# Kernel tuning notes

Hardware: AMD Instinct MI355X
Metric: run time of the kernel (lower is better)

The kernel has to match this reference:

```python
import jax, jax.numpy as jnp
import numpy as np

OUT_C, K, Z_DIM = 256, 64 and 64, 3  # placeholder; real constants below
OUT_C = 256
K = 3
Z_DIM = 64
B, H, W = 16, 128, 128


def setup_inputs() -> dict:
    key = jax.random.key(0)
    k1, k2, k3 = jax.random.split(key, 3)
    x = jax.random.normal(k1, (B, OUT_C, H, W), dtype=jnp.float32)
    z = jax.random.normal(k2, (B, Z_DIM), dtype=jnp.float32)
    # nn.Linear(z_dim, out_c*k*k, bias=False) weight: (out_c*k*k, z_dim)
    W_lin = jax.random.normal(k3, (OUT_C * K * K, Z_DIM), dtype=jnp.float32) * 0.05
    return {"x": x, "z": z, "W_lin": W_lin}


def reference(x, z, W_lin):
    # Hypernetwork: per-sample depthwise kernels, (B, out_c, 1, k, k)
    W_dw = (z @ W_lin.T).reshape(B, OUT_C, 1, K, K)
    pad = K // 2

    def conv_one(xi, wi):
        # xi: (C,H,W), wi: (out_c,1,k,k); depthwise conv, groups=out_c==C
        return jax.lax.conv_general_dilated(
            xi[None],  # (1,C,H,W)
            wi,
            window_strides=(1, 1),
            padding=[(pad, pad), (pad, pad)],
            dimension_numbers=("NCHW", "OIHW", "NCHW"),
            feature_group_count=OUT_C,
        )[0]

    return jax.vmap(conv_one)(x, W_dw)  # (B, out_c, H, W)
```

## Files before the change

### kernel.cpp

```cpp
#include <hip/hip_runtime.h>
#include <hip/hip_bf16.h>

#define BATCH   16
#define OUT_C   256
#define KK      3
#define Z_DIM   64
#define H_DIM   128
#define W_DIM   128

typedef float vf4 __attribute__((ext_vector_type(4)));

__global__ void hyper_gemm_kernel(const float* __restrict__ z,
                                  const float* __restrict__ W_lin,
                                  float* __restrict__ wdw) {
    const int tid = blockIdx.x * blockDim.x + threadIdx.x;
    const int total = BATCH * OUT_C * KK * KK;
    if (tid >= total) return;
    const int b = tid / (OUT_C * KK * KK);
    const int j = tid - b * (OUT_C * KK * KK);

    const vf4* zr = reinterpret_cast<const vf4*>(z + b * Z_DIM);
    const vf4* wr = reinterpret_cast<const vf4*>(W_lin + (size_t)j * Z_DIM);

    float acc = 0.f;
#pragma unroll
    for (int i = 0; i < Z_DIM / 4; ++i) {
        vf4 a = zr[i];
        vf4 w = wr[i];
        acc += a.x * w.x + a.y * w.y + a.z * w.z + a.w * w.w;
    }
    wdw[tid] = acc;
}

__global__ __launch_bounds__(256)
void dwconv3x3_kernel(const float* __restrict__ x,
                      const float* __restrict__ wdw,
                      float* __restrict__ out) {
    const int slab  = blockIdx.x & 1;
    const int plane = blockIdx.x >> 1;

    const float* __restrict__ xin  = x   + (size_t)plane * (H_DIM * W_DIM);
    float*       __restrict__ oout = out + (size_t)plane * (H_DIM * W_DIM);

    const float* __restrict__ wp = wdw + (size_t)plane * (KK * KK);
    const float w00 = wp[0], w01 = wp[1], w02 = wp[2];
    const float w10 = wp[3], w11 = wp[4], w12 = wp[5];
    const float w20 = wp[6], w21 = wp[7], w22 = wp[8];

    const int tcol = threadIdx.x & 31;
    const int trow = threadIdx.x >> 5;
    const int c0   = tcol * 4;
    const int r0   = slab * 64 + trow * 8;

    vf4 raw[10];
#pragma unroll
    for (int i = 0; i < 10; ++i) {
        const int ir  = r0 - 1 + i;
        const int irc = ir < 0 ? 0 : (ir > H_DIM - 1 ? H_DIM - 1 : ir);
        raw[i] = *reinterpret_cast<const vf4*>(xin + irc * W_DIM + c0);
    }
    __builtin_amdgcn_sched_barrier(0);

    vf4   m[10];
    float lft[10], rgt[10];
#pragma unroll
    for (int i = 0; i < 10; ++i) {
        const int ir = r0 - 1 + i;
        const float msk = (ir >= 0 && ir < H_DIM) ? 1.f : 0.f;
        m[i] = raw[i] * msk;
        const float tl = __shfl_up(m[i].w, 1);
        const float tr = __shfl_down(m[i].x, 1);
        lft[i] = (tcol == 0)  ? 0.f : tl;
        rgt[i] = (tcol == 31) ? 0.f : tr;
    }

#pragma unroll
    for (int j = 0; j < 8; ++j) {
        const float A[6] = { lft[j],     m[j].x,     m[j].y,     m[j].z,     m[j].w,     rgt[j]     };
        const float B[6] = { lft[j + 1], m[j + 1].x, m[j + 1].y, m[j + 1].z, m[j + 1].w, rgt[j + 1] };
        const float C[6] = { lft[j + 2], m[j + 2].x, m[j + 2].y, m[j + 2].z, m[j + 2].w, rgt[j + 2] };

        vf4 s;
        float o[4];
#pragma unroll
        for (int k = 0; k < 4; ++k) {
            float a;
            a = fmaf(w00, A[k], fmaf(w01, A[k + 1], w02 * A[k + 2]));
            a = fmaf(w10, B[k], fmaf(w11, B[k + 1], fmaf(w12, B[k + 2], a)));
            a = fmaf(w20, C[k], fmaf(w21, C[k + 1], fmaf(w22, C[k + 2], a)));
            o[k] = a;
        }
        s.x = o[0]; s.y = o[1]; s.z = o[2]; s.w = o[3];
        __builtin_nontemporal_store(
            s, reinterpret_cast<vf4*>(oout + (r0 + j) * W_DIM + c0));
    }
}

extern "C" void kernel_launch(void* const* d_in, const int* in_sizes, int n_in,
                              void* d_out, int out_size, void* d_ws, size_t ws_size,
                              hipStream_t stream) {
    const float* x     = (const float*)d_in[0];
    const float* z     = (const float*)d_in[1];
    const float* W_lin = (const float*)d_in[2];
    float* out = (float*)d_out;
    float* wdw = (float*)d_ws;

    {
        const int total = BATCH * OUT_C * KK * KK;
        const int blk = 256;
        hyper_gemm_kernel<<<(total + blk - 1) / blk, blk, 0, stream>>>(z, W_lin, wdw);
    }

    {
        const int grid = BATCH * OUT_C * 2;
        dwconv3x3_kernel<<<grid, 256, 0, stream>>>(x, wdw, out);
    }
}
```

Before: 87.01 us.

## Fuse hypernetwork weight GEMV into depthwise conv kernel via wavefront reductions

```diff
diff --git a/kernel.cpp b/kernel.cpp
--- a/kernel.cpp
+++ b/kernel.cpp
@@ -10,42 +10,18 @@
 
 typedef float vf4 __attribute__((ext_vector_type(4)));
 
-__global__ void hyper_gemm_kernel(const float* __restrict__ z,
-                                  const float* __restrict__ W_lin,
-                                  float* __restrict__ wdw) {
-    const int tid = blockIdx.x * blockDim.x + threadIdx.x;
-    const int total = BATCH * OUT_C * KK * KK;
-    if (tid >= total) return;
-    const int b = tid / (OUT_C * KK * KK);
-    const int j = tid - b * (OUT_C * KK * KK);
-
-    const vf4* zr = reinterpret_cast<const vf4*>(z + b * Z_DIM);
-    const vf4* wr = reinterpret_cast<const vf4*>(W_lin + (size_t)j * Z_DIM);
-
-    float acc = 0.f;
-#pragma unroll
-    for (int i = 0; i < Z_DIM / 4; ++i) {
-        vf4 a = zr[i];
-        vf4 w = wr[i];
-        acc += a.x * w.x + a.y * w.y + a.z * w.z + a.w * w.w;
-    }
-    wdw[tid] = acc;
-}
-
 __global__ __launch_bounds__(256)
-void dwconv3x3_kernel(const float* __restrict__ x,
-                      const float* __restrict__ wdw,
-                      float* __restrict__ out) {
+void dwconv3x3_fused_kernel(const float* __restrict__ x,
+                            const float* __restrict__ z,
+                            const float* __restrict__ W_lin,
+                            float* __restrict__ out) {
     const int slab  = blockIdx.x & 1;
     const int plane = blockIdx.x >> 1;
+    const int b     = plane >> 8;
+    const int c     = plane & 255;
 
     const float* __restrict__ xin  = x   + (size_t)plane * (H_DIM * W_DIM);
     float*       __restrict__ oout = out + (size_t)plane * (H_DIM * W_DIM);
-
-    const float* __restrict__ wp = wdw + (size_t)plane * (KK * KK);
-    const float w00 = wp[0], w01 = wp[1], w02 = wp[2];
-    const float w10 = wp[3], w11 = wp[4], w12 = wp[5];
-    const float w20 = wp[6], w21 = wp[7], w22 = wp[8];
 
     const int tcol = threadIdx.x & 31;
     const int trow = threadIdx.x >> 5;
@@ -60,6 +36,21 @@
         raw[i] = *reinterpret_cast<const vf4*>(xin + irc * W_DIM + c0);
     }
     __builtin_amdgcn_sched_barrier(0);
+
+    const int lane = threadIdx.x & 63;
+    const float zv = z[b * Z_DIM + lane];
+    float wsum[9];
+#pragma unroll
+    for (int j = 0; j < 9; ++j) {
+        float p = zv * W_lin[(size_t)(c * (KK * KK) + j) * Z_DIM + lane];
+#pragma unroll
+        for (int off = 32; off; off >>= 1)
+            p += __shfl_xor(p, off);
+        wsum[j] = p;
+    }
+    const float w00 = wsum[0], w01 = wsum[1], w02 = wsum[2];
+    const float w10 = wsum[3], w11 = wsum[4], w12 = wsum[5];
+    const float w20 = wsum[6], w21 = wsum[7], w22 = wsum[8];
 
     vf4   m[10];
     float lft[10], rgt[10];
@@ -103,16 +94,7 @@
     const float* z     = (const float*)d_in[1];
     const float* W_lin = (const float*)d_in[2];
     float* out = (float*)d_out;
-    float* wdw = (float*)d_ws;
 
-    {
-        const int total = BATCH * OUT_C * KK * KK;
-        const int blk = 256;
-        hyper_gemm_kernel<<<(total + blk - 1) / blk, blk, 0, stream>>>(z, W_lin, wdw);
-    }
-
-    {
-        const int grid = BATCH * OUT_C * 2;
-        dwconv3x3_kernel<<<grid, 256, 0, stream>>>(x, wdw, out);
-    }
+    const int grid = BATCH * OUT_C * 2;
+    dwconv3x3_fused_kernel<<<grid, 256, 0, stream>>>(x, z, W_lin, out);
 }
```

New measurement: 82.51 us. -5.2%, faster.
